# Performance work log

Measured on AMD Instinct MI355X. Metric: run time of the kernel, lower is better.

Reference implementation:

```python
import jax, jax.numpy as jnp
import numpy as np

DIM_OUT = 64


def setup_inputs() -> dict:
    key = jax.random.key(0)
    k1, k2, k3, k4 = jax.random.split(key, 4)
    B, N, D_in, D_out = 4, 4096, 512, DIM_OUT
    x = jax.random.normal(k1, (B, N, D_in), dtype=jnp.float32)
    s = 1.0 / np.sqrt(D_in)
    Wk = jax.random.normal(k2, (D_out, D_in), dtype=jnp.float32) * s
    Wq = jax.random.normal(k3, (D_out, D_in), dtype=jnp.float32) * s
    Wv = jax.random.normal(k4, (D_out, D_in), dtype=jnp.float32) * s
    return {"x": x, "Wk": Wk, "Wq": Wq, "Wv": Wv}


def reference(x, Wk, Wq, Wv):
    # x: [B, N, D_in]; W*: [D_out, D_in] (torch Linear, no bias -> x @ W.T)
    keys = jnp.einsum('bnd,od->bno', x, Wk)
    queries = jnp.einsum('bnd,od->bno', x, Wq)
    values = jnp.einsum('bnd,od->bno', x, Wv)
    d_out = Wk.shape[0]
    # causal attention scores: [B, N, N]
    scores = jnp.einsum('bio,bjo->bij', queries, keys) / jnp.sqrt(jnp.float32(d_out))
    N = x.shape[1]
    causal = jnp.tril(jnp.ones((N, N), dtype=bool))  # [N, N]
    scores = jnp.where(causal[None, :, :], scores, -jnp.inf)
    att = jax.nn.softmax(scores, axis=-1)
    return jnp.einsum('bjo,bij->bio', values, att)
```

## Files before the change

### kernel.cpp

```cpp
#include <hip/hip_runtime.h>
#include <hip/hip_bf16.h>
#include <math.h>

#define N_   4096
#define DIN  512
#define D_   64

typedef __attribute__((ext_vector_type(8))) short  bf16x8;
typedef __attribute__((ext_vector_type(4))) float  f32x4;

#define ZERO4 ((f32x4){0.f, 0.f, 0.f, 0.f})

__device__ __forceinline__ unsigned short bf16rne(float x) {
    unsigned u = __float_as_uint(x);
    return (unsigned short)((u + 0x7FFFu + ((u >> 16) & 1u)) >> 16);
}
__device__ __forceinline__ unsigned cvt2(float a, float b) {
    __hip_bfloat162 h = __float22bfloat162_rn(make_float2(a, b));
    unsigned u; __builtin_memcpy(&u, &h, 4);
    return u;
}
__device__ __forceinline__ uint2 cvt4(float4 v) {
    return make_uint2(cvt2(v.x, v.y), cvt2(v.z, v.w));
}
__device__ __forceinline__ int swz(int row, int byte_in_row) {
    return (row * 128 + (byte_in_row ^ ((row & 7) << 4))) >> 1;
}

#define GLD16(gp, lp)                                                          \
    __builtin_amdgcn_global_load_lds(                                          \
        (const __attribute__((address_space(1))) unsigned int*)(gp),           \
        (__attribute__((address_space(3))) unsigned int*)(lp), 16, 0, 0)

__device__ __forceinline__ int pb128(int qi) {
    const int g = qi >> 2, r = qi & 3;
    return qi + 2 * g * (g - 1) + r * g;
}
#define PART128_F 8320

__global__ __launch_bounds__(512) void proj_kernel(
    const float* __restrict__ X, const float* __restrict__ Wk,
    const float* __restrict__ Wq, const float* __restrict__ Wv,
    unsigned short* __restrict__ Kb, unsigned short* __restrict__ Qb,
    unsigned short* __restrict__ Vt)
{
    __shared__ unsigned short Xs[2][64 * 64];
    __shared__ unsigned short Ws[2][192 * 64];

    const int tid  = threadIdx.x;
    const int lane = tid & 63;
    const int w    = tid >> 6;
    const int q15  = lane & 15;
    const int hi   = lane >> 4;
    const int rt   = w >> 1;
    const int oh   = w & 1;
    const int rbase = blockIdx.x * 64;

    float4 xr[2], wr[6];

    auto loadT = [&](int kc) {
        #pragma unroll
        for (int i = 0; i < 2; ++i) {
            const int idx = tid + i * 512;
            xr[i] = *(const float4*)(X + (size_t)(rbase + (idx >> 4)) * DIN + kc + (idx & 15) * 4);
        }
        #pragma unroll
        for (int i = 0; i < 6; ++i) {
            const int idx  = tid + i * 512;
            const int wrow = idx >> 4;
            const float* Wp = (wrow < 64)  ? Wk + (size_t)wrow * DIN
                            : (wrow < 128) ? Wq + (size_t)(wrow - 64) * DIN
                                           : Wv + (size_t)(wrow - 128) * DIN;
            wr[i] = *(const float4*)(Wp + kc + (idx & 15) * 4);
        }
    };
    auto storeT = [&](int p) {
        #pragma unroll
        for (int i = 0; i < 2; ++i) {
            const int idx = tid + i * 512;
            *(uint2*)&Xs[p][swz(idx >> 4, (idx & 15) * 8)] = cvt4(xr[i]);
        }
        #pragma unroll
        for (int i = 0; i < 6; ++i) {
            const int idx = tid + i * 512;
            *(uint2*)&Ws[p][swz(idx >> 4, (idx & 15) * 8)] = cvt4(wr[i]);
        }
    };

    f32x4 acc[6];
    #pragma unroll
    for (int i = 0; i < 6; ++i) acc[i] = ZERO4;

    loadT(0);
    int p = 0;
    for (int it = 0; it < 8; ++it) {
        storeT(p);
        __syncthreads();
        if (it < 7) loadT((it + 1) * 64);
        #pragma unroll
        for (int ks = 0; ks < 2; ++ks) {
            bf16x8 af = *(const bf16x8*)&Xs[p][swz(rt * 16 + q15, ks * 64 + hi * 16)];
            #pragma unroll
            for (int j = 0; j < 6; ++j) {
                bf16x8 bfr = *(const bf16x8*)&Ws[p][swz((oh * 6 + j) * 16 + q15, ks * 64 + hi * 16)];
                acc[j] = __builtin_amdgcn_mfma_f32_16x16x32_bf16(af, bfr, acc[j], 0, 0, 0);
            }
        }
        p ^= 1;
    }

    unsigned short* Os = &Ws[0][0];
    #pragma unroll
    for (int j = 0; j < 6; ++j) {
        const int og = oh * 6 + j;
        #pragma unroll
        for (int r = 0; r < 4; ++r) {
            const int n = rt * 16 + hi * 4 + r;
            const int o = og * 16 + q15;
            unsigned short v = bf16rne(acc[j][r]);
            if (og < 4)      Kb[(size_t)(rbase + n) * D_ + o]        = v;
            else if (og < 8) Qb[(size_t)(rbase + n) * D_ + (o - 64)] = v;
            else             Os[n * 66 + (o - 128)]                  = v;
        }
    }
    __syncthreads();
    {
        const int o  = tid >> 3;
        const int ng = (tid & 7) * 8;
        unsigned short tmp[8];
        #pragma unroll
        for (int i = 0; i < 8; ++i) tmp[i] = Os[(ng + i) * 66 + o];
        const int b  = rbase >> 12;
        const int nb = rbase & (N_ - 1);
        *(uint4*)(Vt + ((size_t)b * D_ + o) * N_ + nb + ng) = *(uint4*)&tmp[0];
    }
}

__global__ __launch_bounds__(256) void attn_part_kernel(
    const unsigned short* __restrict__ Qb, const unsigned short* __restrict__ Kb,
    const unsigned short* __restrict__ Vt, float* __restrict__ Pws)
{
    __shared__ unsigned short Ks[2][64 * 64];
    __shared__ unsigned short Vs[2][64 * 64];
    __shared__ unsigned short Pb[4][32 * 64];

    const int tid  = threadIdx.x;
    const int lane = tid & 63;
    const int w    = tid >> 6;
    const int q15  = lane & 15;
    const int hi   = lane >> 4;

    const int b = blockIdx.x & 3;
    const int u = blockIdx.x >> 2;
    const int v = 143 - u;
    int g = 0;
    #pragma unroll
    for (int t = 0; t < 7; ++t)
        if (2 * (t + 1) * (t + 2) <= v) g = t + 1;
    const int idx = v - 2 * g * (g + 1);
    const int qs  = idx / (g + 1);
    const int qi  = 4 * g + qs;
    const int sl  = idx - qs * (g + 1);

    const int nch  = 2 * qi + 2;
    const int cbeg = sl * 8;
    const int cend = min(nch, cbeg + 8);
    const int qb   = qi * 128;

    const unsigned short* Qp = Qb + (size_t)b * N_ * D_;
    const unsigned short* Kp = Kb + (size_t)b * N_ * D_;
    const unsigned short* Vp = Vt + (size_t)b * D_ * N_;

    bf16x8 qf[2][2];
    #pragma unroll
    for (int qq = 0; qq < 2; ++qq)
        #pragma unroll
        for (int ks = 0; ks < 2; ++ks)
            qf[qq][ks] = *(const bf16x8*)(Qp + (size_t)(qb + w * 32 + qq * 16 + q15) * D_ + ks * 32 + hi * 8);

    f32x4 accO[2][4];
    #pragma unroll
    for (int qq = 0; qq < 2; ++qq)
        #pragma unroll
        for (int dt = 0; dt < 4; ++dt) accO[qq][dt] = ZERO4;
    float lsum[2] = {0.f, 0.f};

    const int lsw = 8 * ((lane & 7) ^ (lane >> 3));

    auto issueChunk = [&](int p, int c) {
        const int kb2 = c * 64;
        #pragma unroll
        for (int i = 0; i < 2; ++i) {
            const int r8  = w * 2 + i;
            const int row = r8 * 8 + (lane >> 3);
            GLD16(Kp + (size_t)(kb2 + row) * D_ + lsw, &Ks[p][r8 * 512]);
            GLD16(Vp + (size_t)row * N_ + kb2 + lsw,   &Vs[p][r8 * 512]);
        }
    };

    issueChunk(0, cbeg);
    __syncthreads();

    unsigned short* Pw = &Pb[w][0];
    const float SC = 0.125f * 1.44269504f;
    int p = 0;

    for (int c = cbeg; c < cend; ++c) {
        if (c + 1 < cend) issueChunk(p ^ 1, c + 1);
        const int kbase = c * 64;
        const bool edge = (c >= nch - 2);

        f32x4 sv[2][4];
        #pragma unroll
        for (int kt = 0; kt < 4; ++kt) {
            bf16x8 k0 = *(const bf16x8*)&Ks[p][swz(kt * 16 + q15, hi * 16)];
            bf16x8 k1 = *(const bf16x8*)&Ks[p][swz(kt * 16 + q15, 64 + hi * 16)];
            sv[0][kt] = __builtin_amdgcn_mfma_f32_16x16x32_bf16(k0, qf[0][0], ZERO4, 0, 0, 0);
            sv[0][kt] = __builtin_amdgcn_mfma_f32_16x16x32_bf16(k1, qf[0][1], sv[0][kt], 0, 0, 0);
            sv[1][kt] = __builtin_amdgcn_mfma_f32_16x16x32_bf16(k0, qf[1][0], ZERO4, 0, 0, 0);
            sv[1][kt] = __builtin_amdgcn_mfma_f32_16x16x32_bf16(k1, qf[1][1], sv[1][kt], 0, 0, 0);
        }

        #pragma unroll
        for (int qq = 0; qq < 2; ++qq) {
            const int qg = qb + w * 32 + qq * 16 + q15;
            #pragma unroll
            for (int kt = 0; kt < 4; ++kt) {
                float pv[4];
                #pragma unroll
                for (int r = 0; r < 4; ++r) {
                    float vv = sv[qq][kt][r] * SC;
                    const int kg = kbase + kt * 16 + hi * 4 + r;
                    if (edge) vv = (kg <= qg) ? vv : -INFINITY;
                    pv[r] = __builtin_amdgcn_exp2f(vv);
                    lsum[qq] += pv[r];
                }
                *(uint2*)&Pw[swz(qq * 16 + q15, kt * 32 + hi * 8)] =
                    make_uint2(cvt2(pv[0], pv[1]), cvt2(pv[2], pv[3]));
            }
        }

        #pragma unroll
        for (int ks2 = 0; ks2 < 2; ++ks2) {
            bf16x8 vf[4];
            #pragma unroll
            for (int dt = 0; dt < 4; ++dt)
                vf[dt] = *(const bf16x8*)&Vs[p][swz(dt * 16 + q15, ks2 * 64 + hi * 16)];
            #pragma unroll
            for (int qq = 0; qq < 2; ++qq) {
                bf16x8 pf = *(const bf16x8*)&Pw[swz(qq * 16 + q15, ks2 * 64 + hi * 16)];
                #pragma unroll
                for (int dt = 0; dt < 4; ++dt)
                    accO[qq][dt] = __builtin_amdgcn_mfma_f32_16x16x32_bf16(vf[dt], pf, accO[qq][dt], 0, 0, 0);
            }
        }

        __syncthreads();
        p ^= 1;
    }

    #pragma unroll
    for (int qq = 0; qq < 2; ++qq) {
        lsum[qq] += __shfl_xor(lsum[qq], 16);
        lsum[qq] += __shfl_xor(lsum[qq], 32);
    }

    float* partO = Pws + ((size_t)b * 144 + pb128(qi) + sl) * PART128_F;
    #pragma unroll
    for (int qq = 0; qq < 2; ++qq) {
        #pragma unroll
        for (int dt = 0; dt < 4; ++dt)
            #pragma unroll
            for (int r = 0; r < 4; ++r)
                partO[(dt * 16 + hi * 4 + r) * 128 + w * 32 + qq * 16 + q15] = accO[qq][dt][r];
        if (hi == 0) partO[8192 + w * 32 + qq * 16 + q15] = lsum[qq];
    }
}

__global__ __launch_bounds__(256) void attn_merge_kernel(
    const float* __restrict__ Pws, float* __restrict__ O)
{
    __shared__ float Tr[64 * 132];
    __shared__ float Ls[128];

    const int tid = threadIdx.x;
    const int b   = blockIdx.x & 3;
    const int qi  = blockIdx.x >> 2;
    const int np  = (qi >> 2) + 1;
    const float* base = Pws + ((size_t)b * 144 + pb128(qi)) * PART128_F;

    {
        const int d  = tid >> 2;
        const int qg = (tid & 3) * 32;
        float s[32];
        #pragma unroll
        for (int i = 0; i < 32; ++i) s[i] = 0.f;
        for (int pp = 0; pp < np; ++pp) {
            const float* sp = base + (size_t)pp * PART128_F + d * 128 + qg;
            #pragma unroll
            for (int i = 0; i < 8; ++i) {
                float4 v = *(const float4*)(sp + i * 4);
                s[4*i]   += v.x; s[4*i+1] += v.y;
                s[4*i+2] += v.z; s[4*i+3] += v.w;
            }
        }
        #pragma unroll
        for (int i = 0; i < 32; ++i) Tr[d * 132 + qg + i] = s[i];
    }
    if (tid < 128) {
        float L = 0.f;
        for (int pp = 0; pp < np; ++pp) L += base[(size_t)pp * PART128_F + 8192 + tid];
        Ls[tid] = 1.0f / L;
    }
    __syncthreads();
    {
        const int q  = tid >> 1;
        const int dg = (tid & 1) * 32;
        const float rL = Ls[q];
        float* dst = O + ((size_t)b * N_ + qi * 128 + q) * D_ + dg;
        #pragma unroll
        for (int i = 0; i < 8; ++i) {
            float4 v = make_float4(Tr[(dg + 4*i    ) * 132 + q] * rL,
                                   Tr[(dg + 4*i + 1) * 132 + q] * rL,
                                   Tr[(dg + 4*i + 2) * 132 + q] * rL,
                                   Tr[(dg + 4*i + 3) * 132 + q] * rL);
            *(float4*)(dst + i * 4) = v;
        }
    }
}

extern "C" void kernel_launch(void* const* d_in, const int* in_sizes, int n_in,
                              void* d_out, int out_size, void* d_ws, size_t ws_size,
                              hipStream_t stream)
{
    const float* x  = (const float*)d_in[0];
    const float* Wk = (const float*)d_in[1];
    const float* Wq = (const float*)d_in[2];
    const float* Wv = (const float*)d_in[3];
    float* O = (float*)d_out;

    const size_t per = (size_t)4 * N_ * D_;
    unsigned short* Kb = (unsigned short*)d_ws;
    unsigned short* Qb = Kb + per;
    unsigned short* Vt = Qb + per;
    float* Pws = (float*)((char*)d_ws + 3 * per * sizeof(unsigned short));

    proj_kernel<<<dim3(4 * N_ / 64), 512, 0, stream>>>(x, Wk, Wq, Wv, Kb, Qb, Vt);
    attn_part_kernel<<<dim3(576), 256, 0, stream>>>(Qb, Kb, Vt, Pws);
    attn_merge_kernel<<<dim3(128), 256, 0, stream>>>(Pws, O);
}
```

Before: 56.93 us.

## Keep softmax probabilities in registers via permlane swaps, drop LDS staging

The exp'd score fragments are no longer written to a per-wave LDS buffer and read back as the MFMA operand. They are rearranged in registers with v_permlane32/16 swaps into the A-operand layout, and the P·V MFMA operands are swapped so the output comes out query-major. The partial output layout becomes row-major, which lets the merge kernel drop its LDS transpose and __syncthreads and read and write contiguous rows directly. This removes LDS traffic and a sync in exchange for inline asm permlane ops that depend on the exact lane layout.

Measured after the change: 55.31 us. 1.03x faster.

```diff
diff --git a/kernel.cpp b/kernel.cpp
--- a/kernel.cpp
+++ b/kernel.cpp
@@ -22,6 +22,12 @@
 }
 __device__ __forceinline__ uint2 cvt4(float4 v) {
     return make_uint2(cvt2(v.x, v.y), cvt2(v.z, v.w));
+}
+__device__ __forceinline__ void pl32swap(unsigned &a, unsigned &b) {
+    asm volatile("v_permlane32_swap_b32 %0, %1" : "+v"(a), "+v"(b));
+}
+__device__ __forceinline__ void pl16swap(unsigned &a, unsigned &b) {
+    asm volatile("v_permlane16_swap_b32 %0, %1" : "+v"(a), "+v"(b));
 }
 __device__ __forceinline__ int swz(int row, int byte_in_row) {
     return (row * 128 + (byte_in_row ^ ((row & 7) << 4))) >> 1;
@@ -142,7 +148,6 @@
 {
     __shared__ unsigned short Ks[2][64 * 64];
     __shared__ unsigned short Vs[2][64 * 64];
-    __shared__ unsigned short Pb[4][32 * 64];
 
     const int tid  = threadIdx.x;
     const int lane = tid & 63;
@@ -201,7 +206,6 @@
     issueChunk(0, cbeg);
     __syncthreads();
 
-    unsigned short* Pw = &Pb[w][0];
     const float SC = 0.125f * 1.44269504f;
     int p = 0;
 
@@ -224,6 +228,7 @@
         #pragma unroll
         for (int qq = 0; qq < 2; ++qq) {
             const int qg = qb + w * 32 + qq * 16 + q15;
+            unsigned pk[4][2];
             #pragma unroll
             for (int kt = 0; kt < 4; ++kt) {
                 float pv[4];
@@ -235,23 +240,25 @@
                     pv[r] = __builtin_amdgcn_exp2f(vv);
                     lsum[qq] += pv[r];
                 }
-                *(uint2*)&Pw[swz(qq * 16 + q15, kt * 32 + hi * 8)] =
-                    make_uint2(cvt2(pv[0], pv[1]), cvt2(pv[2], pv[3]));
+                pk[kt][0] = cvt2(pv[0], pv[1]);
+                pk[kt][1] = cvt2(pv[2], pv[3]);
             }
-        }
-
-        #pragma unroll
-        for (int ks2 = 0; ks2 < 2; ++ks2) {
-            bf16x8 vf[4];
             #pragma unroll
-            for (int dt = 0; dt < 4; ++dt)
-                vf[dt] = *(const bf16x8*)&Vs[p][swz(dt * 16 + q15, ks2 * 64 + hi * 16)];
-            #pragma unroll
-            for (int qq = 0; qq < 2; ++qq) {
-                bf16x8 pf = *(const bf16x8*)&Pw[swz(qq * 16 + q15, ks2 * 64 + hi * 16)];
+            for (int ks2 = 0; ks2 < 2; ++ks2) {
+                unsigned a0 = pk[2 * ks2][0],     a1 = pk[2 * ks2][1];
+                unsigned b0 = pk[2 * ks2 + 1][0], b1 = pk[2 * ks2 + 1][1];
+                pl32swap(a0, b0);
+                pl32swap(a1, b1);
+                pl16swap(a0, b0);
+                pl16swap(a1, b1);
+                unsigned pw[4] = {a0, a1, b0, b1};
+                bf16x8 pa;
+                __builtin_memcpy(&pa, pw, 16);
                 #pragma unroll
-                for (int dt = 0; dt < 4; ++dt)
-                    accO[qq][dt] = __builtin_amdgcn_mfma_f32_16x16x32_bf16(vf[dt], pf, accO[qq][dt], 0, 0, 0);
+                for (int dt = 0; dt < 4; ++dt) {
+                    bf16x8 vf = *(const bf16x8*)&Vs[p][swz(dt * 16 + q15, ks2 * 64 + hi * 16)];
+                    accO[qq][dt] = __builtin_amdgcn_mfma_f32_16x16x32_bf16(pa, vf, accO[qq][dt], 0, 0, 0);
+                }
             }
         }
 
@@ -272,7 +279,7 @@
         for (int dt = 0; dt < 4; ++dt)
             #pragma unroll
             for (int r = 0; r < 4; ++r)
-                partO[(dt * 16 + hi * 4 + r) * 128 + w * 32 + qq * 16 + q15] = accO[qq][dt][r];
+                partO[(w * 32 + qq * 16 + hi * 4 + r) * 64 + dt * 16 + q15] = accO[qq][dt][r];
         if (hi == 0) partO[8192 + w * 32 + qq * 16 + q15] = lsum[qq];
     }
 }
@@ -280,53 +287,35 @@
 __global__ __launch_bounds__(256) void attn_merge_kernel(
     const float* __restrict__ Pws, float* __restrict__ O)
 {
-    __shared__ float Tr[64 * 132];
-    __shared__ float Ls[128];
-
     const int tid = threadIdx.x;
     const int b   = blockIdx.x & 3;
     const int qi  = blockIdx.x >> 2;
     const int np  = (qi >> 2) + 1;
     const float* base = Pws + ((size_t)b * 144 + pb128(qi)) * PART128_F;
 
-    {
-        const int d  = tid >> 2;
-        const int qg = (tid & 3) * 32;
-        float s[32];
-        #pragma unroll
-        for (int i = 0; i < 32; ++i) s[i] = 0.f;
-        for (int pp = 0; pp < np; ++pp) {
-            const float* sp = base + (size_t)pp * PART128_F + d * 128 + qg;
-            #pragma unroll
-            for (int i = 0; i < 8; ++i) {
-                float4 v = *(const float4*)(sp + i * 4);
-                s[4*i]   += v.x; s[4*i+1] += v.y;
-                s[4*i+2] += v.z; s[4*i+3] += v.w;
-            }
-        }
-        #pragma unroll
-        for (int i = 0; i < 32; ++i) Tr[d * 132 + qg + i] = s[i];
-    }
-    if (tid < 128) {
-        float L = 0.f;
-        for (int pp = 0; pp < np; ++pp) L += base[(size_t)pp * PART128_F + 8192 + tid];
-        Ls[tid] = 1.0f / L;
-    }
-    __syncthreads();
-    {
-        const int q  = tid >> 1;
-        const int dg = (tid & 1) * 32;
-        const float rL = Ls[q];
-        float* dst = O + ((size_t)b * N_ + qi * 128 + q) * D_ + dg;
+    const int q  = tid >> 1;
+    const int dg = (tid & 1) * 32;
+
+    float s[32];
+    #pragma unroll
+    for (int i = 0; i < 32; ++i) s[i] = 0.f;
+    float L = 0.f;
+    for (int pp = 0; pp < np; ++pp) {
+        const float* sp = base + (size_t)pp * PART128_F + q * 64 + dg;
         #pragma unroll
         for (int i = 0; i < 8; ++i) {
-            float4 v = make_float4(Tr[(dg + 4*i    ) * 132 + q] * rL,
-                                   Tr[(dg + 4*i + 1) * 132 + q] * rL,
-                                   Tr[(dg + 4*i + 2) * 132 + q] * rL,
-                                   Tr[(dg + 4*i + 3) * 132 + q] * rL);
-            *(float4*)(dst + i * 4) = v;
-        }
-    }
+            float4 v = *(const float4*)(sp + i * 4);
+            s[4*i]   += v.x; s[4*i+1] += v.y;
+            s[4*i+2] += v.z; s[4*i+3] += v.w;
+        }
+        L += base[(size_t)pp * PART128_F + 8192 + q];
+    }
+    const float rL = 1.0f / L;
+    float* dst = O + ((size_t)b * N_ + qi * 128 + q) * D_ + dg;
+    #pragma unroll
+    for (int i = 0; i < 8; ++i)
+        *(float4*)(dst + i * 4) = make_float4(s[4*i] * rL, s[4*i+1] * rL,
+                                              s[4*i+2] * rL, s[4*i+3] * rL);
 }
 
 extern "C" void kernel_launch(void* const* d_in, const int* in_sizes, int n_in,
```
